# Performance work log

Measured on AMD Instinct MI355X. Metric: run time of the kernel, lower is better.

Reference implementation:

```python
import jax, jax.numpy as jnp
import numpy as np


def setup_inputs() -> dict:
    key = jax.random.key(0)
    k1, k2, k3 = jax.random.split(key, 3)
    B, S, K, N = 4, 2048, 4096, 4096
    x = jax.random.normal(k1, (B, S, K), dtype=jnp.float32)
    weight = jax.random.normal(k2, (N, K), dtype=jnp.float32)
    bias = jax.random.normal(k3, (N,), dtype=jnp.float32)
    return {"x": x, "weight": weight, "bias": bias}


def reference(x, weight, bias):
    # --- weight: symmetric per-channel INT8 quantize (channel_dim=0) then dequantize ---
    w_absmax = jnp.max(jnp.abs(weight), axis=1, keepdims=True)          # [N, 1]
    w_scales = jnp.maximum(w_absmax / 127.0, 1e-5)                      # clamp(min=1e-5)
    w_q = jnp.clip(jnp.round(weight / w_scales), -128.0, 127.0)         # integer-valued fp32 (== int8 round-trip)
    w_deq = w_q * w_scales                                              # [N, K]
    # --- activation: symmetric per-tensor INT8 quantize then dequantize ---
    # NOTE: per-tensor branch in the source has NO scale clamp.
    x_scale = jnp.max(jnp.abs(x)) / 127.0
    x_q = jnp.clip(jnp.round(x / x_scale), -128.0, 127.0)
    x_deq = x_q * x_scale                                               # [B, S, K]
    # --- F.linear: x @ W^T + b ---
    out = jnp.einsum('bsk,nk->bsn', x_deq, w_deq) + bias
    return out
```

## Files before the change

### kernel.cpp

```cpp
#include <hip/hip_runtime.h>
#include <stdint.h>

typedef int v4i __attribute__((ext_vector_type(4)));

#define BM 128
#define BN 128
#define BK 64

#define WS_WSCALE_OFF 64
#define WS_XQ_OFF 32768

__device__ __forceinline__ float fmax4abs(float4 v) {
  return fmaxf(fmaxf(fabsf(v.x), fabsf(v.y)), fmaxf(fabsf(v.z), fabsf(v.w)));
}

__global__ __launch_bounds__(256) void absmax_kernel(const float4* __restrict__ x4,
                                                     unsigned* __restrict__ out, int n4) {
  float m = 0.f;
  for (int i = blockIdx.x * blockDim.x + threadIdx.x; i < n4; i += gridDim.x * blockDim.x) {
    m = fmaxf(m, fmax4abs(x4[i]));
  }
  #pragma unroll
  for (int off = 32; off > 0; off >>= 1) m = fmaxf(m, __shfl_down(m, off));
  __shared__ float sm[4];
  if ((threadIdx.x & 63) == 0) sm[threadIdx.x >> 6] = m;
  __syncthreads();
  if (threadIdx.x == 0) {
    m = fmaxf(fmaxf(sm[0], sm[1]), fmaxf(sm[2], sm[3]));
    atomicMax(out, __float_as_uint(m));
  }
}

__global__ __launch_bounds__(256) void wquant_kernel(const float* __restrict__ w,
                                                     char* __restrict__ wq,
                                                     float* __restrict__ wscale, int K) {
  const int n = blockIdx.x;
  const float4* row = (const float4*)(w + (size_t)n * K);
  const int K4 = K >> 2;
  float m = 0.f;
  for (int i = threadIdx.x; i < K4; i += blockDim.x) m = fmaxf(m, fmax4abs(row[i]));
  #pragma unroll
  for (int off = 32; off > 0; off >>= 1) m = fmaxf(m, __shfl_xor(m, off));
  __shared__ float sm[4];
  if ((threadIdx.x & 63) == 0) sm[threadIdx.x >> 6] = m;
  __syncthreads();
  m = fmaxf(fmaxf(sm[0], sm[1]), fmaxf(sm[2], sm[3]));
  const float scale = fmaxf(m / 127.f, 1e-5f);
  if (threadIdx.x == 0) wscale[n] = scale;
  const float inv = 1.f / scale;
  char4* qrow = (char4*)(wq + (size_t)n * K);
  for (int i = threadIdx.x; i < K4; i += blockDim.x) {
    float4 v = row[i];
    char4 q;
    q.x = (char)(int)fminf(fmaxf(rintf(v.x * inv), -128.f), 127.f);
    q.y = (char)(int)fminf(fmaxf(rintf(v.y * inv), -128.f), 127.f);
    q.z = (char)(int)fminf(fmaxf(rintf(v.z * inv), -128.f), 127.f);
    q.w = (char)(int)fminf(fmaxf(rintf(v.w * inv), -128.f), 127.f);
    qrow[i] = q;
  }
}

__global__ __launch_bounds__(256) void xquant_kernel(const float4* __restrict__ x4,
                                                     char4* __restrict__ xq,
                                                     const unsigned* __restrict__ am, int n4) {
  const float scale = __uint_as_float(*am) / 127.f;
  const float inv = 1.f / scale;
  for (int i = blockIdx.x * blockDim.x + threadIdx.x; i < n4; i += gridDim.x * blockDim.x) {
    float4 v = x4[i];
    char4 q;
    q.x = (char)(int)fminf(fmaxf(rintf(v.x * inv), -128.f), 127.f);
    q.y = (char)(int)fminf(fmaxf(rintf(v.y * inv), -128.f), 127.f);
    q.z = (char)(int)fminf(fmaxf(rintf(v.z * inv), -128.f), 127.f);
    q.w = (char)(int)fminf(fmaxf(rintf(v.w * inv), -128.f), 127.f);
    xq[i] = q;
  }
}

__device__ __forceinline__ void gload16(const void* g, void* l) {
  __builtin_amdgcn_global_load_lds((const __attribute__((address_space(1))) void*)g,
                                   (__attribute__((address_space(3))) void*)l, 16, 0, 0);
}

__global__ __launch_bounds__(256) void gemm_i8_kernel(
    const char* __restrict__ Aq, const char* __restrict__ Bq,
    const float* __restrict__ wscale, const float* __restrict__ bias,
    const unsigned* __restrict__ am, float* __restrict__ out,
    int M, int N, int K) {
  __shared__ char As[BM * BK];
  __shared__ char Bs[BN * BK];
  const int tid = threadIdx.x;
  const int lane = tid & 63;
  const int wave = tid >> 6;
  const int wm = wave >> 1, wn = wave & 1;
  const int brow = blockIdx.y * BM;
  const int bcol = blockIdx.x * BN;

  const char* aSrc0 = Aq + (size_t)(brow + (tid >> 2)) * K + (tid & 3) * 16;
  const char* aSrc1 = aSrc0 + (size_t)64 * K;
  const char* bSrc0 = Bq + (size_t)(bcol + (tid >> 2)) * K + (tid & 3) * 16;
  const char* bSrc1 = bSrc0 + (size_t)64 * K;
  char* aDst0 = &As[tid * 16];
  char* aDst1 = &As[4096 + tid * 16];
  char* bDst0 = &Bs[tid * 16];
  char* bDst1 = &Bs[4096 + tid * 16];

  v4i acc[4][4];
  #pragma unroll
  for (int i = 0; i < 4; ++i)
    #pragma unroll
    for (int j = 0; j < 4; ++j) acc[i][j] = (v4i)0;

  const int arow = wm * 64 + (lane & 15);
  const int brow_f = wn * 64 + (lane & 15);
  const int koff = (lane >> 4) * 16;

  for (int k0 = 0; k0 < K; k0 += BK) {
    gload16(aSrc0 + k0, aDst0);
    gload16(aSrc1 + k0, aDst1);
    gload16(bSrc0 + k0, bDst0);
    gload16(bSrc1 + k0, bDst1);
    __syncthreads();

    v4i a[4], b[4];
    #pragma unroll
    for (int mi = 0; mi < 4; ++mi)
      a[mi] = *(const v4i*)&As[(arow + mi * 16) * BK + koff];
    #pragma unroll
    for (int ni = 0; ni < 4; ++ni)
      b[ni] = *(const v4i*)&Bs[(brow_f + ni * 16) * BK + koff];

    #pragma unroll
    for (int mi = 0; mi < 4; ++mi)
      #pragma unroll
      for (int ni = 0; ni < 4; ++ni)
        acc[mi][ni] = __builtin_amdgcn_mfma_i32_16x16x64_i8(a[mi], b[ni], acc[mi][ni], 0, 0, 0);
    __syncthreads();
  }

  const float xscale = __uint_as_float(*am) / 127.f;
  #pragma unroll
  for (int ni = 0; ni < 4; ++ni) {
    const int n = bcol + wn * 64 + ni * 16 + (lane & 15);
    const float sc = xscale * wscale[n];
    const float bs = bias[n];
    #pragma unroll
    for (int mi = 0; mi < 4; ++mi) {
      const int mbase = brow + wm * 64 + mi * 16 + (lane >> 4) * 4;
      #pragma unroll
      for (int r = 0; r < 4; ++r)
        out[(size_t)(mbase + r) * N + n] = (float)acc[mi][ni][r] * sc + bs;
    }
  }
}

extern "C" void kernel_launch(void* const* d_in, const int* in_sizes, int n_in,
                              void* d_out, int out_size, void* d_ws, size_t ws_size,
                              hipStream_t stream) {
  const float* x = (const float*)d_in[0];
  const float* weight = (const float*)d_in[1];
  const float* bias = (const float*)d_in[2];
  float* out = (float*)d_out;

  const int M = 8192, N = 4096, K = 4096;

  char* ws = (char*)d_ws;
  unsigned* am = (unsigned*)ws;
  float* wscale = (float*)(ws + WS_WSCALE_OFF);
  char* xq = ws + WS_XQ_OFF;
  char* wq = ws + WS_XQ_OFF + (size_t)M * K;

  hipMemsetAsync(am, 0, 64, stream);

  const int n4 = (M * K) >> 2;
  absmax_kernel<<<2048, 256, 0, stream>>>((const float4*)x, am, n4);
  wquant_kernel<<<N, 256, 0, stream>>>(weight, wq, wscale, K);
  xquant_kernel<<<2048, 256, 0, stream>>>((const float4*)x, (char4*)xq, am, n4);

  dim3 grid(N / BN, M / BM);
  gemm_i8_kernel<<<grid, 256, 0, stream>>>(xq, wq, wscale, bias, am, out, M, N, K);
}
```

Baseline: 486.5 us.

## Rewrite int8 GEMM as 256x256 tile, 4-stage LDS pipeline with swizzle

Replaces the 128x128 single-buffered int8 MFMA GEMM with a 512-thread, 256x256-tile kernel that keeps four 32 KB LDS stages and prefetches three k-steps ahead using explicit vmcnt waits. It XOR-swizzles the LDS layout to avoid bank conflicts, splits each k-step into two MFMA phases with setprio, and remaps block IDs for L2 locality. The absmax and weight-quantize kernels are also merged into one launch. This aims to hide global-load latency and raise MFMA utilization, at the cost of 128 KB of LDS, one block per CU, and hardcoded sizes (NT=64, 512 blocks).

Result: faster. 442.6 us (-9.0%).

```diff
diff --git a/kernel.cpp b/kernel.cpp
--- a/kernel.cpp
+++ b/kernel.cpp
@@ -3,10 +3,6 @@
 
 typedef int v4i __attribute__((ext_vector_type(4)));
 
-#define BM 128
-#define BN 128
-#define BK 64
-
 #define WS_WSCALE_OFF 64
 #define WS_XQ_OFF 32768
 
@@ -14,49 +10,48 @@
   return fmaxf(fmaxf(fabsf(v.x), fabsf(v.y)), fmaxf(fabsf(v.z), fabsf(v.w)));
 }
 
-__global__ __launch_bounds__(256) void absmax_kernel(const float4* __restrict__ x4,
-                                                     unsigned* __restrict__ out, int n4) {
-  float m = 0.f;
-  for (int i = blockIdx.x * blockDim.x + threadIdx.x; i < n4; i += gridDim.x * blockDim.x) {
-    m = fmaxf(m, fmax4abs(x4[i]));
-  }
-  #pragma unroll
-  for (int off = 32; off > 0; off >>= 1) m = fmaxf(m, __shfl_down(m, off));
+__global__ __launch_bounds__(256) void prep_kernel(const float4* __restrict__ x4, int n4,
+                                                   unsigned* __restrict__ am,
+                                                   const float* __restrict__ w,
+                                                   char* __restrict__ wq,
+                                                   float* __restrict__ wscale, int K) {
   __shared__ float sm[4];
-  if ((threadIdx.x & 63) == 0) sm[threadIdx.x >> 6] = m;
-  __syncthreads();
-  if (threadIdx.x == 0) {
+  if (blockIdx.x < 2048) {
+    float m = 0.f;
+    for (int i = blockIdx.x * blockDim.x + threadIdx.x; i < n4; i += 2048 * blockDim.x)
+      m = fmaxf(m, fmax4abs(x4[i]));
+    #pragma unroll
+    for (int off = 32; off > 0; off >>= 1) m = fmaxf(m, __shfl_down(m, off));
+    if ((threadIdx.x & 63) == 0) sm[threadIdx.x >> 6] = m;
+    __syncthreads();
+    if (threadIdx.x == 0) {
+      m = fmaxf(fmaxf(sm[0], sm[1]), fmaxf(sm[2], sm[3]));
+      atomicMax(am, __float_as_uint(m));
+    }
+  } else {
+    const int n = blockIdx.x - 2048;
+    const float4* row = (const float4*)(w + (size_t)n * K);
+    const int K4 = K >> 2;
+    float m = 0.f;
+    for (int i = threadIdx.x; i < K4; i += blockDim.x) m = fmaxf(m, fmax4abs(row[i]));
+    #pragma unroll
+    for (int off = 32; off > 0; off >>= 1) m = fmaxf(m, __shfl_xor(m, off));
+    if ((threadIdx.x & 63) == 0) sm[threadIdx.x >> 6] = m;
+    __syncthreads();
     m = fmaxf(fmaxf(sm[0], sm[1]), fmaxf(sm[2], sm[3]));
-    atomicMax(out, __float_as_uint(m));
-  }
-}
-
-__global__ __launch_bounds__(256) void wquant_kernel(const float* __restrict__ w,
-                                                     char* __restrict__ wq,
-                                                     float* __restrict__ wscale, int K) {
-  const int n = blockIdx.x;
-  const float4* row = (const float4*)(w + (size_t)n * K);
-  const int K4 = K >> 2;
-  float m = 0.f;
-  for (int i = threadIdx.x; i < K4; i += blockDim.x) m = fmaxf(m, fmax4abs(row[i]));
-  #pragma unroll
-  for (int off = 32; off > 0; off >>= 1) m = fmaxf(m, __shfl_xor(m, off));
-  __shared__ float sm[4];
-  if ((threadIdx.x & 63) == 0) sm[threadIdx.x >> 6] = m;
-  __syncthreads();
-  m = fmaxf(fmaxf(sm[0], sm[1]), fmaxf(sm[2], sm[3]));
-  const float scale = fmaxf(m / 127.f, 1e-5f);
-  if (threadIdx.x == 0) wscale[n] = scale;
-  const float inv = 1.f / scale;
-  char4* qrow = (char4*)(wq + (size_t)n * K);
-  for (int i = threadIdx.x; i < K4; i += blockDim.x) {
-    float4 v = row[i];
-    char4 q;
-    q.x = (char)(int)fminf(fmaxf(rintf(v.x * inv), -128.f), 127.f);
-    q.y = (char)(int)fminf(fmaxf(rintf(v.y * inv), -128.f), 127.f);
-    q.z = (char)(int)fminf(fmaxf(rintf(v.z * inv), -128.f), 127.f);
-    q.w = (char)(int)fminf(fmaxf(rintf(v.w * inv), -128.f), 127.f);
-    qrow[i] = q;
+    const float scale = fmaxf(m / 127.f, 1e-5f);
+    if (threadIdx.x == 0) wscale[n] = scale;
+    const float inv = 1.f / scale;
+    char4* qrow = (char4*)(wq + (size_t)n * K);
+    for (int i = threadIdx.x; i < K4; i += blockDim.x) {
+      float4 v = row[i];
+      char4 q;
+      q.x = (char)(int)fminf(fmaxf(rintf(v.x * inv), -128.f), 127.f);
+      q.y = (char)(int)fminf(fmaxf(rintf(v.y * inv), -128.f), 127.f);
+      q.z = (char)(int)fminf(fmaxf(rintf(v.z * inv), -128.f), 127.f);
+      q.w = (char)(int)fminf(fmaxf(rintf(v.w * inv), -128.f), 127.f);
+      qrow[i] = q;
+    }
   }
 }
 
@@ -81,74 +76,110 @@
                                    (__attribute__((address_space(3))) void*)l, 16, 0, 0);
 }
 
-__global__ __launch_bounds__(256) void gemm_i8_kernel(
+#define NT 64
+
+__global__ __launch_bounds__(512, 1) void gemm_i8_8p(
     const char* __restrict__ Aq, const char* __restrict__ Bq,
     const float* __restrict__ wscale, const float* __restrict__ bias,
     const unsigned* __restrict__ am, float* __restrict__ out,
     int M, int N, int K) {
-  __shared__ char As[BM * BK];
-  __shared__ char Bs[BN * BK];
+  extern __shared__ char smem[];
   const int tid = threadIdx.x;
   const int lane = tid & 63;
   const int wave = tid >> 6;
-  const int wm = wave >> 1, wn = wave & 1;
-  const int brow = blockIdx.y * BM;
-  const int bcol = blockIdx.x * BN;
-
-  const char* aSrc0 = Aq + (size_t)(brow + (tid >> 2)) * K + (tid & 3) * 16;
-  const char* aSrc1 = aSrc0 + (size_t)64 * K;
-  const char* bSrc0 = Bq + (size_t)(bcol + (tid >> 2)) * K + (tid & 3) * 16;
-  const char* bSrc1 = bSrc0 + (size_t)64 * K;
-  char* aDst0 = &As[tid * 16];
-  char* aDst1 = &As[4096 + tid * 16];
-  char* bDst0 = &Bs[tid * 16];
-  char* bDst1 = &Bs[4096 + tid * 16];
-
-  v4i acc[4][4];
+  const int wm = wave >> 2;
+  const int wn = wave & 3;
+
+  const int bid = blockIdx.x;
+  const int swz = (bid & 7) * 64 + (bid >> 3);
+  const int brow = (swz >> 4) * 256;
+  const int bcol = (swz & 15) * 256;
+
+  const int srow = tid >> 2;
+  const int scol = ((tid & 3) ^ (srow & 3)) * 16;
+  const char* aS0 = Aq + (size_t)(brow + srow) * K + scol;
+  const char* aS1 = aS0 + (size_t)128 * K;
+  const char* bS0 = Bq + (size_t)(bcol + srow) * K + scol;
+  const char* bS1 = bS0 + (size_t)128 * K;
+
+  const int rswz = ((lane >> 4) ^ (lane & 3)) * 16;
+  const int aRd = (wm * 128 + (lane & 15)) * 64 + rswz;
+  const int bRd = (wn * 64 + (lane & 15)) * 64 + rswz;
+
+  v4i acc[8][4];
   #pragma unroll
-  for (int i = 0; i < 4; ++i)
+  for (int i = 0; i < 8; ++i)
     #pragma unroll
     for (int j = 0; j < 4; ++j) acc[i][j] = (v4i)0;
 
-  const int arow = wm * 64 + (lane & 15);
-  const int brow_f = wn * 64 + (lane & 15);
-  const int koff = (lane >> 4) * 16;
-
-  for (int k0 = 0; k0 < K; k0 += BK) {
-    gload16(aSrc0 + k0, aDst0);
-    gload16(aSrc1 + k0, aDst1);
-    gload16(bSrc0 + k0, bDst0);
-    gload16(bSrc1 + k0, bDst1);
-    __syncthreads();
-
+  #pragma unroll
+  for (int pt = 0; pt < 3; ++pt) {
+    char* bufN = smem + pt * 32768;
+    gload16(aS0 + pt * 64, bufN + tid * 16);
+    gload16(aS1 + pt * 64, bufN + 8192 + tid * 16);
+    gload16(bS0 + pt * 64, bufN + 16384 + tid * 16);
+    gload16(bS1 + pt * 64, bufN + 16384 + 8192 + tid * 16);
+  }
+
+  for (int t = 0; t < NT; ++t) {
+    if (t < NT - 2)      asm volatile("s_waitcnt vmcnt(8)" ::: "memory");
+    else if (t == NT - 2) asm volatile("s_waitcnt vmcnt(4)" ::: "memory");
+    else                 asm volatile("s_waitcnt vmcnt(0)" ::: "memory");
+    __builtin_amdgcn_s_barrier();
+
+    const char* bufA = smem + (t & 3) * 32768;
+    char* bufN = smem + ((t + 3) & 3) * 32768;
+
+    if (t + 3 < NT) {
+      gload16(aS0 + (t + 3) * 64, bufN + tid * 16);
+      gload16(aS1 + (t + 3) * 64, bufN + 8192 + tid * 16);
+    }
     v4i a[4], b[4];
     #pragma unroll
-    for (int mi = 0; mi < 4; ++mi)
-      a[mi] = *(const v4i*)&As[(arow + mi * 16) * BK + koff];
-    #pragma unroll
-    for (int ni = 0; ni < 4; ++ni)
-      b[ni] = *(const v4i*)&Bs[(brow_f + ni * 16) * BK + koff];
-
-    #pragma unroll
-    for (int mi = 0; mi < 4; ++mi)
+    for (int nf = 0; nf < 4; ++nf)
+      b[nf] = *(const v4i*)(bufA + 16384 + bRd + nf * 1024);
+    #pragma unroll
+    for (int mf = 0; mf < 4; ++mf)
+      a[mf] = *(const v4i*)(bufA + aRd + mf * 1024);
+    __builtin_amdgcn_s_barrier();
+    __builtin_amdgcn_s_setprio(1);
+    #pragma unroll
+    for (int mf = 0; mf < 4; ++mf)
       #pragma unroll
-      for (int ni = 0; ni < 4; ++ni)
-        acc[mi][ni] = __builtin_amdgcn_mfma_i32_16x16x64_i8(a[mi], b[ni], acc[mi][ni], 0, 0, 0);
-    __syncthreads();
+      for (int nf = 0; nf < 4; ++nf)
+        acc[mf][nf] = __builtin_amdgcn_mfma_i32_16x16x64_i8(a[mf], b[nf], acc[mf][nf], 0, 0, 0);
+    __builtin_amdgcn_s_setprio(0);
+    __builtin_amdgcn_s_barrier();
+
+    if (t + 3 < NT) {
+      gload16(bS0 + (t + 3) * 64, bufN + 16384 + tid * 16);
+      gload16(bS1 + (t + 3) * 64, bufN + 16384 + 8192 + tid * 16);
+    }
+    #pragma unroll
+    for (int mf = 0; mf < 4; ++mf)
+      a[mf] = *(const v4i*)(bufA + aRd + (mf + 4) * 1024);
+    __builtin_amdgcn_s_barrier();
+    __builtin_amdgcn_s_setprio(1);
+    #pragma unroll
+    for (int mf = 0; mf < 4; ++mf)
+      #pragma unroll
+      for (int nf = 0; nf < 4; ++nf)
+        acc[mf + 4][nf] = __builtin_amdgcn_mfma_i32_16x16x64_i8(a[mf], b[nf], acc[mf + 4][nf], 0, 0, 0);
+    __builtin_amdgcn_s_setprio(0);
   }
 
   const float xscale = __uint_as_float(*am) / 127.f;
   #pragma unroll
-  for (int ni = 0; ni < 4; ++ni) {
-    const int n = bcol + wn * 64 + ni * 16 + (lane & 15);
+  for (int nf = 0; nf < 4; ++nf) {
+    const int n = bcol + wn * 64 + nf * 16 + (lane & 15);
     const float sc = xscale * wscale[n];
     const float bs = bias[n];
     #pragma unroll
-    for (int mi = 0; mi < 4; ++mi) {
-      const int mbase = brow + wm * 64 + mi * 16 + (lane >> 4) * 4;
+    for (int mf = 0; mf < 8; ++mf) {
+      const int mbase = brow + wm * 128 + mf * 16 + (lane >> 4) * 4;
       #pragma unroll
       for (int r = 0; r < 4; ++r)
-        out[(size_t)(mbase + r) * N + n] = (float)acc[mi][ni][r] * sc + bs;
+        out[(size_t)(mbase + r) * N + n] = (float)acc[mf][nf][r] * sc + bs;
     }
   }
 }
@@ -172,10 +203,10 @@
   hipMemsetAsync(am, 0, 64, stream);
 
   const int n4 = (M * K) >> 2;
-  absmax_kernel<<<2048, 256, 0, stream>>>((const float4*)x, am, n4);
-  wquant_kernel<<<N, 256, 0, stream>>>(weight, wq, wscale, K);
+  prep_kernel<<<2048 + N, 256, 0, stream>>>((const float4*)x, n4, am, weight, wq, wscale, K);
   xquant_kernel<<<2048, 256, 0, stream>>>((const float4*)x, (char4*)xq, am, n4);
 
-  dim3 grid(N / BN, M / BM);
-  gemm_i8_kernel<<<grid, 256, 0, stream>>>(xq, wq, wscale, bias, am, out, M, N, K);
-}
+  (void)hipFuncSetAttribute(reinterpret_cast<const void*>(gemm_i8_8p),
+                            hipFuncAttributeMaxDynamicSharedMemorySize, 131072);
+  gemm_i8_8p<<<512, 512, 131072, stream>>>(xq, wq, wscale, bias, am, out, M, N, K);
+}
```
